# Kernel optimization log

Measured on AMD Instinct MI355X. Metric: run time of the kernel, lower is better.

The kernel has to match this reference:

```python
import jax, jax.numpy as jnp
import numpy as np

NEG = -1000000.0


def setup_inputs() -> dict:
    key = jax.random.key(0)
    k0, k1, k2, k3, k4 = jax.random.split(key, 5)
    b, c, h, w = 4, 256, 64, 64
    dvt_c = 768
    x = jax.random.normal(k0, (b, c, h, w), jnp.float32)
    dvtfeats = jax.random.normal(k1, (b, dvt_c, h, w), jnp.float32)
    coarse = (jax.random.uniform(k2, (b, 1, h, w)) > 0.5).astype(jnp.float32)
    mask = jnp.repeat(jnp.repeat(coarse, 8, axis=2), 8, axis=3)  # [b,1,512,512]
    # K_conv: Conv2d(c+768 -> c, 1x1) with bias; fuse: Conv2d(2c -> c, 1x1) no bias
    K_w = jax.random.normal(k3, (c, c + dvt_c), jnp.float32) * 0.02
    K_b = jnp.zeros((c,), jnp.float32)
    fuse_w = jax.random.normal(k4, (c, 2 * c), jnp.float32) * 0.02
    return {"x": x, "mask": mask, "dvtfeats": dvtfeats, "K_w": K_w, "K_b": K_b, "fuse_w": fuse_w}


def _conv1x1(inp, w, b=None):
    out = jnp.einsum('bihw,oi->bohw', inp, w)
    if b is not None:
        out = out + b[None, :, None, None]
    return out


def _forward(x, mask, dvtfeats, K_w, K_b, fuse_w):
    b, c, h, w = x.shape
    n = h * w
    # maxpool(8,8) then binarize
    m = mask.reshape(b, 1, h, 8, w, 8).max(axis=(3, 5))
    m = (m > 0).astype(x.dtype)            # [b,1,h,w] foreground mask
    bm = 1.0 - m                            # background mask
    # K_conv applied once (original applies the same conv twice to the same input)
    feats = _conv1x1(jnp.concatenate([x, dvtfeats], axis=1), K_w, K_b)  # [b,c,h,w]
    K = (feats * bm).reshape(b, c, n)
    Q = (feats * m).reshape(b, c, n).transpose(0, 2, 1)  # [b,n,c]
    K = K / (jnp.linalg.norm(K, axis=1, keepdims=True) + 1e-8)
    Q = Q / (jnp.linalg.norm(Q, axis=2, keepdims=True) + 1e-8)
    V = (x * bm).reshape(b, c, n)
    score = jnp.einsum('bqc,bck->bqk', Q, K) * 20.0       # [b,n,n] cosine sims
    qm = m.reshape(b, 1, n)    # query mask (foreground)
    km = bm.reshape(b, 1, n)   # key mask (background)
    score = score + (1.0 - km) * NEG + (1.0 - qm).transpose(0, 2, 1) * NEG
    att = jax.nn.softmax(score, axis=-1)
    att = att * qm.transpose(0, 2, 1) * km                # zero out invalid rows/cols
    # att_fore[b,c,q] = sum_k V[b,c,k] * att[b,q,k]
    att_fore = jnp.einsum('bck,bqk->bcq', V, att).reshape(b, c, h, w)
    fused = _conv1x1(jnp.concatenate([att_fore, x], axis=1), fuse_w)
    visatt = att.sum(axis=1).reshape(b, 1, h, w)          # sum over query dim
    attmask = jnp.repeat(jnp.repeat(visatt, 8, axis=2), 8, axis=3)  # nearest upsample x8
    attmask = attmask / attmask.max()
    out = fused * m + x * (1.0 - m)
    return out, attmask


def reference(x, mask, dvtfeats, K_w, K_b, fuse_w):
    return _forward(x, mask, dvtfeats, K_w, K_b, fuse_w)
```

## Files before the change

### kernel.cpp

```cpp
#include <hip/hip_runtime.h>
#include <hip/hip_bf16.h>

typedef __attribute__((ext_vector_type(8))) short short8;
typedef __attribute__((ext_vector_type(4))) float f32x4;
typedef unsigned int uint;
typedef unsigned short ushort;

constexpr int BATCH = 4;
constexpr int CH    = 256;
constexpr int N     = 4096;
constexpr int DVC   = 768;
constexpr int CIN   = 1024;
constexpr int KC    = 512;
constexpr int PBS   = 5 * 1024 * 1024;
constexpr int QCH   = 32;
constexpr int SPLITK = 4;

constexpr size_t OFF_M    = 0;
constexpr size_t OFF_INV  = 64ull << 10;
constexpr size_t OFF_VIS  = 128ull << 10;
constexpr size_t OFF_MAXV = 192ull << 10;
constexpr size_t OFF_CNT  = 196ull << 10;
constexpr size_t OFF_FGI  = 256ull << 10;
constexpr size_t OFF_BGI  = 320ull << 10;
constexpr size_t OFF_P2S  = 384ull << 10;
constexpr size_t OFF_KMC  = 448ull << 10;
constexpr size_t OFF_PART = 1ull << 20;
constexpr size_t OFF_KWB  = 5ull << 20;
constexpr size_t OFF_FWB  = OFF_KWB + (512ull << 10);
constexpr size_t OFF_XT   = 6ull << 20;
constexpr size_t OFF_QC   = 38ull << 20;
constexpr size_t OFF_KCC  = 46ull << 20;
constexpr size_t OFF_XC   = 54ull << 20;
constexpr size_t OFF_AFT  = 62ull << 20;
constexpr size_t OFF_P    = 70ull << 20;
constexpr size_t OFF_AFP  = 110ull << 20;

__device__ __forceinline__ ushort f2bf(float f) {
    __hip_bfloat16 h = __float2bfloat16(f);
    return __builtin_bit_cast(ushort, h);
}
__device__ __forceinline__ float bf2f(ushort u) {
    uint v = (uint)u << 16;
    return __builtin_bit_cast(float, v);
}

typedef const __attribute__((address_space(1))) uint* gptr_t;
typedef __attribute__((address_space(3))) uint* lptr_t;
__device__ __forceinline__ void gload_lds16(const void* g, void* l) {
    __builtin_amdgcn_global_load_lds((gptr_t)g, (lptr_t)l, 16, 0, 0);
}

template<int WM, int WN>
__device__ __forceinline__ void gemm_core(
    const ushort* __restrict__ A0, int lda, int m0,
    const ushort* __restrict__ B0, int ldb0, int kend0,
    const ushort* __restrict__ B1, int ldb1,
    int n0, int K,
    ushort* AsL, ushort* BsL, f32x4 acc[4][4])
{
    constexpr int NW = WM * WN, BM = WM * 64, BN = WN * 64;
    const int t = threadIdx.x, lane = t & 63, wid = t >> 6;
    const int wm = (wid / WN) * 64, wn = (wid % WN) * 64;

    for (int k0 = 0; k0 < K; k0 += 64) {
        #pragma unroll
        for (int c = wid; c < BM / 8; c += NW) {
            const ushort* g = A0 + (size_t)(m0 + c * 8 + (lane >> 3)) * lda + (k0 + (lane & 7) * 8);
            gload_lds16(g, AsL + c * 512);
        }
        const ushort* Bsrc = (k0 < kend0) ? B0 : B1;
        const int ldb = (k0 < kend0) ? ldb0 : ldb1;
        const int kc  = (k0 < kend0) ? k0 : (k0 - kend0);
        #pragma unroll
        for (int c = wid; c < BN / 8; c += NW) {
            const ushort* g = Bsrc + (size_t)(n0 + c * 8 + (lane >> 3)) * ldb + (kc + (lane & 7) * 8);
            gload_lds16(g, BsL + c * 512);
        }
        __syncthreads();

        const int ra = wm + (lane & 15), rb = wn + (lane & 15), ko = (lane >> 4) * 8;
        #pragma unroll
        for (int kk = 0; kk < 64; kk += 32) {
            short8 a[4], b[4];
            #pragma unroll
            for (int i = 0; i < 4; i++) a[i] = *(const short8*)(AsL + (ra + i * 16) * 64 + kk + ko);
            #pragma unroll
            for (int j = 0; j < 4; j++) b[j] = *(const short8*)(BsL + (rb + j * 16) * 64 + kk + ko);
            #pragma unroll
            for (int i = 0; i < 4; i++)
                #pragma unroll
                for (int j = 0; j < 4; j++)
                    acc[i][j] = __builtin_amdgcn_mfma_f32_16x16x32_bf16(a[i], b[j], acc[i][j], 0, 0, 0);
        }
        __syncthreads();
    }
}

__device__ __forceinline__ void zero_acc(f32x4 acc[4][4]) {
    f32x4 z = {0.f, 0.f, 0.f, 0.f};
    #pragma unroll
    for (int i = 0; i < 4; i++)
        #pragma unroll
        for (int j = 0; j < 4; j++) acc[i][j] = z;
}

__global__ __launch_bounds__(256) void k_prep_tr(
    const float* __restrict__ mask, const float* __restrict__ Kw,
    const float* __restrict__ fw, const float* __restrict__ x,
    float* __restrict__ m, float* __restrict__ vis, uint* __restrict__ maxv,
    ushort* __restrict__ Kwb, ushort* __restrict__ fwb, ushort* __restrict__ xT)
{
    __shared__ float Ls[64][65];
    const int bid = blockIdx.x;
    const int t = threadIdx.x;
    if (bid < 64) {
        int idx = bid * 256 + t;
        int b = idx >> 12, p = idx & 4095;
        int y = p >> 6, xx = p & 63;
        const float* base = mask + (size_t)b * 512 * 512 + (y * 8) * 512 + xx * 8;
        float mx = 0.f;
        for (int dy = 0; dy < 8; dy++) {
            #pragma unroll
            for (int dx = 0; dx < 8; dx++) mx = fmaxf(mx, base[dy * 512 + dx]);
        }
        m[idx] = (mx > 0.f) ? 1.f : 0.f;
        vis[idx] = 0.f;
        if (idx == 0) maxv[0] = 0u;
    } else if (bid < 1600) {
        int i = (bid - 64) * 256 + t;
        if (i < CH * CIN) Kwb[i] = f2bf(Kw[i]);
        else              fwb[i - CH * CIN] = f2bf(fw[i - CH * CIN]);
    } else {
        const int tr_id = bid - 1600;
        const int ci0 = (tr_id & 3) * 64;
        const int n0 = ((tr_id >> 2) & 63) * 64;
        const int b = tr_id >> 8;
        const float* s = x + (size_t)b * CH * 4096;
        #pragma unroll
        for (int it = 0; it < 4; it++) {
            int f4 = it * 256 + t;
            int r = f4 >> 4, c4 = f4 & 15;
            float4 v = *(const float4*)(s + (size_t)(ci0 + r) * 4096 + n0 + c4 * 4);
            Ls[r][c4 * 4 + 0] = v.x; Ls[r][c4 * 4 + 1] = v.y;
            Ls[r][c4 * 4 + 2] = v.z; Ls[r][c4 * 4 + 3] = v.w;
        }
        __syncthreads();
        ushort* d = xT + (size_t)b * 4096 * CH;
        #pragma unroll
        for (int it = 0; it < 8; it++) {
            int p = it * 256 + t;
            int rn = p >> 5, cc2 = p & 31;
            uint val = (uint)f2bf(Ls[cc2 * 2][rn]) | ((uint)f2bf(Ls[cc2 * 2 + 1][rn]) << 16);
            *(uint*)(d + (size_t)(n0 + rn) * CH + ci0 + cc2 * 2) = val;
        }
    }
}

__global__ __launch_bounds__(256) void k_scan(
    const float* __restrict__ m, int* __restrict__ fgi, int* __restrict__ bgi,
    int* __restrict__ counts, float* __restrict__ kmc, int* __restrict__ p2s)
{
    const int b = blockIdx.x, t = threadIdx.x;
    const float* mb = m + (size_t)b * N;
    __shared__ int sfg[256], sbg[256];
    bool isf[16];
    int cf = 0, cb_ = 0;
    #pragma unroll
    for (int j = 0; j < 16; j++) {
        bool f = mb[t * 16 + j] != 0.f;
        isf[j] = f; cf += f ? 1 : 0; cb_ += f ? 0 : 1;
    }
    sfg[t] = cf; sbg[t] = cb_;
    __syncthreads();
    for (int off = 1; off < 256; off <<= 1) {
        int vf = (t >= off) ? sfg[t - off] : 0;
        int vb = (t >= off) ? sbg[t - off] : 0;
        __syncthreads();
        sfg[t] += vf; sbg[t] += vb;
        __syncthreads();
    }
    int basef = sfg[t] - cf, baseb = sbg[t] - cb_;
    int nfg = sfg[255], nbg = sbg[255];
    #pragma unroll
    for (int j = 0; j < 16; j++) {
        int p = t * 16 + j;
        if (isf[j]) { fgi[b * N + basef] = p; p2s[b * N + p] = basef | (1 << 30); basef++; }
        else        { bgi[b * N + baseb] = p; p2s[b * N + p] = baseb; baseb++; }
    }
    if (t == 0) {
        counts[b * 4 + 0] = nfg;
        counts[b * 4 + 1] = (nfg + 127) & ~127;
        counts[b * 4 + 2] = nbg;
        counts[b * 4 + 3] = (nbg + 127) & ~127;
    }
    for (int j = t; j < N; j += 256) kmc[b * N + j] = (j < nbg) ? 1.f : 0.f;
}

__global__ __launch_bounds__(256) void k_feats_vg(
    const ushort* __restrict__ Kwb, const ushort* __restrict__ xT,
    const float* __restrict__ dvt, const float* __restrict__ Kb,
    const int* __restrict__ p2s, const int* __restrict__ bgi,
    const int* __restrict__ counts,
    ushort* __restrict__ Qc, ushort* __restrict__ Kc, ushort* __restrict__ xc)
{
    __shared__ __align__(16) char smem[58624];
    const int bid = blockIdx.x;
    const int t = threadIdx.x, lane = t & 63, wid = t >> 6;

    if (bid >= 256) {
        ushort (*Xs)[264] = (ushort(*)[264])smem;
        const int vid = bid - 256;
        const int b = vid >> 6;
        const int ki0 = (vid & 63) * 64;
        const int nbg = counts[b * 4 + 2], nbgp = counts[b * 4 + 3];
        if (ki0 >= nbgp) return;
        const int j = t >> 2, part = t & 3;
        const int ki = ki0 + j;
        if (ki < nbg) {
            const ushort* src = xT + ((size_t)b * N + bgi[(size_t)b * N + ki]) * CH + part * 64;
            #pragma unroll
            for (int q = 0; q < 8; q++)
                *(uint4*)&Xs[j][part * 64 + q * 8] = *(const uint4*)(src + q * 8);
        } else {
            uint4 z = {0, 0, 0, 0};
            #pragma unroll
            for (int q = 0; q < 8; q++)
                *(uint4*)&Xs[j][part * 64 + q * 8] = z;
        }
        __syncthreads();
        const int c = t;
        ushort* dst = xc + ((size_t)b * CH + c) * N + ki0;
        uint w[32];
        #pragma unroll
        for (int jj = 0; jj < 32; jj++)
            w[jj] = (uint)Xs[2 * jj][c] | ((uint)Xs[2 * jj + 1][c] << 16);
        #pragma unroll
        for (int q = 0; q < 8; q++) {
            uint4 o = { w[q * 4], w[q * 4 + 1], w[q * 4 + 2], w[q * 4 + 3] };
            *(uint4*)(dst + q * 8) = o;
        }
        return;
    }

    ushort* As = (ushort*)smem;
    ushort* Bs = (ushort*)(smem + 32768);
    float (*Ls)[65] = (float(*)[65])(smem + 40960);
    float (*red)[64] = (float(*)[64])(smem + 57600);
    const int b = bid >> 6;
    const int n0 = (bid & 63) * 64;
    const ushort* xTb = xT + (size_t)b * N * CH;
    const float* dvb = dvt + (size_t)b * DVC * N;
    f32x4 acc[4][4]; zero_acc(acc);

    for (int k0 = 0; k0 < 256; k0 += 64) {
        #pragma unroll
        for (int c = wid; c < 32; c += 4)
            gload_lds16(Kwb + (size_t)(c * 8 + (lane >> 3)) * CIN + k0 + (lane & 7) * 8, As + c * 512);
        #pragma unroll
        for (int c = wid; c < 8; c += 4)
            gload_lds16(xTb + (size_t)(n0 + c * 8 + (lane >> 3)) * CH + k0 + (lane & 7) * 8, Bs + c * 512);
        __syncthreads();
        const int ra = wid * 64 + (lane & 15), rb = lane & 15, ko = (lane >> 4) * 8;
        #pragma unroll
        for (int kk = 0; kk < 64; kk += 32) {
            short8 a[4], bb[4];
            #pragma unroll
            for (int i = 0; i < 4; i++) a[i] = *(const short8*)(As + (ra + i * 16) * 64 + kk + ko);
            #pragma unroll
            for (int j = 0; j < 4; j++) bb[j] = *(const short8*)(Bs + (rb + j * 16) * 64 + kk + ko);
            #pragma unroll
            for (int i = 0; i < 4; i++)
                #pragma unroll
                for (int j = 0; j < 4; j++)
                    acc[i][j] = __builtin_amdgcn_mfma_f32_16x16x32_bf16(a[i], bb[j], acc[i][j], 0, 0, 0);
        }
        __syncthreads();
    }
    for (int k0 = 256; k0 < 1024; k0 += 64) {
        #pragma unroll
        for (int c = wid; c < 32; c += 4)
            gload_lds16(Kwb + (size_t)(c * 8 + (lane >> 3)) * CIN + k0 + (lane & 7) * 8, As + c * 512);
        const float* dsrc = dvb + (size_t)(k0 - 256) * N + n0;
        #pragma unroll
        for (int it = 0; it < 4; it++) {
            int f4 = it * 256 + t;
            int r = f4 >> 4, c4 = (f4 & 15) * 4;
            float4 v = *(const float4*)(dsrc + (size_t)r * N + c4);
            Ls[r][c4 + 0] = v.x; Ls[r][c4 + 1] = v.y;
            Ls[r][c4 + 2] = v.z; Ls[r][c4 + 3] = v.w;
        }
        __syncthreads();
        {
            int rn = t >> 2;
            int ks = (t & 3) * 16;
            #pragma unroll
            for (int j2 = 0; j2 < 8; j2++) {
                int kk = ks + j2 * 2;
                uint val = (uint)f2bf(Ls[kk][rn]) | ((uint)f2bf(Ls[kk + 1][rn]) << 16);
                int idx = (rn * 64 + kk) ^ ((rn & 7) << 3);
                *(uint*)(Bs + idx) = val;
            }
        }
        __syncthreads();
        const int ra = wid * 64 + (lane & 15), rb = lane & 15, ko = (lane >> 4) * 8;
        #pragma unroll
        for (int kk = 0; kk < 64; kk += 32) {
            short8 a[4], bb[4];
            #pragma unroll
            for (int i = 0; i < 4; i++) a[i] = *(const short8*)(As + (ra + i * 16) * 64 + kk + ko);
            #pragma unroll
            for (int j = 0; j < 4; j++) {
                int row = rb + j * 16;
                int idx = (row * 64 + kk + ko) ^ ((row & 7) << 3);
                bb[j] = *(const short8*)(Bs + idx);
            }
            #pragma unroll
            for (int i = 0; i < 4; i++)
                #pragma unroll
                for (int j = 0; j < 4; j++)
                    acc[i][j] = __builtin_amdgcn_mfma_f32_16x16x32_bf16(a[i], bb[j], acc[i][j], 0, 0, 0);
        }
        __syncthreads();
    }

    const int wm = wid * 64;
    float sj[4] = {0.f, 0.f, 0.f, 0.f};
    #pragma unroll
    for (int i = 0; i < 4; i++) {
        int mbase = wm + i * 16 + ((lane >> 4) * 4);
        float4 bias = *(const float4*)(Kb + mbase);
        #pragma unroll
        for (int j = 0; j < 4; j++) {
            acc[i][j][0] += bias.x; acc[i][j][1] += bias.y;
            acc[i][j][2] += bias.z; acc[i][j][3] += bias.w;
            sj[j] += acc[i][j][0] * acc[i][j][0] + acc[i][j][1] * acc[i][j][1]
                   + acc[i][j][2] * acc[i][j][2] + acc[i][j][3] * acc[i][j][3];
        }
    }
    #pragma unroll
    for (int j = 0; j < 4; j++) {
        sj[j] += __shfl_xor(sj[j], 16);
        sj[j] += __shfl_xor(sj[j], 32);
    }
    if (lane < 16) {
        #pragma unroll
        for (int j = 0; j < 4; j++) red[wid][j * 16 + lane] = sj[j];
    }
    __syncthreads();
    const int* pb = p2s + (size_t)b * N + n0;
    #pragma unroll
    for (int j = 0; j < 4; j++) {
        int n = j * 16 + (lane & 15);
        float s = red[0][n] + red[1][n] + red[2][n] + red[3][n];
        float invn = 1.f / (sqrtf(s) + 1e-8f);
        int sl = pb[n];
        ushort* dst = (sl & (1 << 30)) ? Qc : Kc;
        int slot = sl & 0x3FFFFFFF;
        ushort* drow = dst + ((size_t)b * N + slot) * CH;
        #pragma unroll
        for (int i = 0; i < 4; i++) {
            int mbase = wm + i * 16 + ((lane >> 4) * 4);
            ushort4 o = { f2bf(acc[i][j][0] * invn), f2bf(acc[i][j][1] * invn),
                          f2bf(acc[i][j][2] * invn), f2bf(acc[i][j][3] * invn) };
            *(ushort4*)(drow + mbase) = o;
        }
    }
}

__global__ __launch_bounds__(128) void k_score(
    const ushort* __restrict__ Qc, const ushort* __restrict__ Kc,
    const float* __restrict__ kmc, const int* __restrict__ counts,
    ushort* __restrict__ P, float* __restrict__ rowpart)
{
    const int b = blockIdx.z;
    const int nfgp = counts[b * 4 + 1], nbgp = counts[b * 4 + 3];
    const int m0 = blockIdx.y * 128;
    const int n0 = blockIdx.x * 64;
    if (m0 >= nfgp || n0 >= nbgp) return;
    __shared__ ushort SH[(128 + 64) * 64];
    const int t = threadIdx.x, lane = t & 63, wid = t >> 6;
    const ushort* Qb = Qc + (size_t)b * N * CH;
    const ushort* Kb_ = Kc + (size_t)b * N * CH;
    f32x4 acc[4][4]; zero_acc(acc);
    gemm_core<2, 1>(Qb, CH, m0, Kb_, CH, CH, Kb_, CH, n0, CH, SH, SH + 128 * 64, acc);

    const int wm = wid * 64;
    float km[4];
    #pragma unroll
    for (int j = 0; j < 4; j++) km[j] = kmc[(size_t)b * N + n0 + j * 16 + (lane & 15)];

    ushort* Cs = SH;
    float sir[4][4] = {};
    #pragma unroll
    for (int i = 0; i < 4; i++) {
        int rbase = wm + i * 16 + ((lane >> 4) * 4);
        #pragma unroll
        for (int j = 0; j < 4; j++) {
            int cl = j * 16 + (lane & 15);
            #pragma unroll
            for (int r = 0; r < 4; r++) {
                float p = (km[j] != 0.f) ? __expf(20.f * acc[i][j][r] - 20.f) : 0.f;
                Cs[(rbase + r) * 64 + cl] = f2bf(p);
                sir[i][r] += p;
            }
        }
    }
    #pragma unroll
    for (int i = 0; i < 4; i++)
        #pragma unroll
        for (int r = 0; r < 4; r++) {
            float s = sir[i][r];
            s += __shfl_xor(s, 1); s += __shfl_xor(s, 2);
            s += __shfl_xor(s, 4); s += __shfl_xor(s, 8);
            sir[i][r] = s;
        }
    if ((lane & 15) == 0) {
        const int sl = n0 >> 6;
        #pragma unroll
        for (int i = 0; i < 4; i++)
            #pragma unroll
            for (int r = 0; r < 4; r++) {
                int row = wm + i * 16 + ((lane >> 4) * 4) + r;
                rowpart[((size_t)b * N + m0 + row) * 64 + sl] = sir[i][r];
            }
    }
    __syncthreads();
    ushort* Pb = P + (size_t)b * PBS;
    #pragma unroll
    for (int it = 0; it < 8; it++) {
        int v8 = it * 128 + t;
        int row = v8 >> 3, c8 = (v8 & 7) * 8;
        *(uint4*)(Pb + (size_t)(m0 + row) * nbgp + n0 + c8) = *(const uint4*)(Cs + row * 64 + c8);
    }
}

__global__ __launch_bounds__(256) void k_att_fore(
    const ushort* __restrict__ xc, const ushort* __restrict__ P,
    const int* __restrict__ counts, ushort* __restrict__ AFp)
{
    const int b = blockIdx.z & (BATCH - 1);
    const int sk = blockIdx.z / BATCH;
    const int nfgp = counts[b * 4 + 1], nbgp = counts[b * 4 + 3];
    const int n0 = blockIdx.x * 64;
    if (n0 >= nfgp) return;
    const int kchunk = ((nbgp / 64 + SPLITK - 1) / SPLITK) * 64;
    const int k0s = sk * kchunk;
    const int len = min(kchunk, nbgp - k0s);

    const int lane = threadIdx.x & 63, wid = threadIdx.x >> 6;
    f32x4 acc[4][4]; zero_acc(acc);
    if (len > 0) {
        __shared__ ushort SH[(256 + 64) * 64];
        const ushort* Pb = P + (size_t)b * PBS + k0s;
        gemm_core<4, 1>(xc + (size_t)b * CH * N + k0s, N, 0,
                        Pb, nbgp, 1 << 30, Pb, nbgp,
                        n0, len, SH, SH + 256 * 64, acc);
    }
    ushort* Ap = AFp + ((size_t)(sk * BATCH + b) * N) * CH;
    const int wm = wid * 64;
    #pragma unroll
    for (int j = 0; j < 4; j++) {
        int qi = n0 + j * 16 + (lane & 15);
        #pragma unroll
        for (int i = 0; i < 4; i++) {
            int mbase = wm + i * 16 + ((lane >> 4) * 4);
            ushort4 o = { f2bf(acc[i][j][0]), f2bf(acc[i][j][1]),
                          f2bf(acc[i][j][2]), f2bf(acc[i][j][3]) };
            *(ushort4*)(Ap + (size_t)qi * CH + mbase) = o;
        }
    }
}

__global__ __launch_bounds__(256) void k_rowaf(
    const float* __restrict__ rowpart, const ushort* __restrict__ AFp,
    const int* __restrict__ fgi, const int* __restrict__ counts,
    float* __restrict__ inv, ushort* __restrict__ AFt)
{
    const int t = threadIdx.x, lane = t & 63, wid = t >> 6;
    const int g = blockIdx.x * 4 + wid;
    const int b = g >> 12, qi = g & 4095;
    const int nfgp = counts[b * 4 + 1], nbgp = counts[b * 4 + 3];
    if (qi >= nfgp) return;
    const int nsl = nbgp >> 6;
    float s = (lane < nsl) ? rowpart[(size_t)g * 64 + lane] : 0.f;
    #pragma unroll
    for (int mm = 1; mm < 64; mm <<= 1) s += __shfl_xor(s, mm);
    float iq = (s > 0.f) ? 1.f / s : 0.f;
    if (lane == 0) inv[g] = iq;
    if (qi < counts[b * 4]) {
        const size_t rowoff = ((size_t)b * N + qi) * CH + lane * 4;
        float s0 = 0.f, s1 = 0.f, s2 = 0.f, s3 = 0.f;
        #pragma unroll
        for (int sk = 0; sk < SPLITK; sk++) {
            ushort4 v = *(const ushort4*)(AFp + (size_t)sk * BATCH * N * CH + rowoff);
            s0 += bf2f(v.x); s1 += bf2f(v.y); s2 += bf2f(v.z); s3 += bf2f(v.w);
        }
        int q = fgi[g];
        ushort4 o = { f2bf(s0 * iq), f2bf(s1 * iq), f2bf(s2 * iq), f2bf(s3 * iq) };
        *(ushort4*)(AFt + ((size_t)b * N + q) * CH + lane * 4) = o;
    }
}

__global__ __launch_bounds__(128) void k_fused(
    const ushort* __restrict__ fwb, const ushort* __restrict__ AFt,
    const ushort* __restrict__ xT, const float* __restrict__ x,
    const float* __restrict__ m_, const float* __restrict__ vis,
    const uint* __restrict__ maxv, float* __restrict__ out,
    float* __restrict__ amask)
{
    __shared__ ushort SH[(64 + 128) * 64];
    const int b = blockIdx.z;
    const int n0 = blockIdx.x * 128, m0 = blockIdx.y * 64;
    const int lane = threadIdx.x & 63, wid = threadIdx.x >> 6;
    const int wn = (wid & 1) * 64;
    f32x4 acc[4][4]; zero_acc(acc);
    gemm_core<1, 2>(fwb, KC, m0,
                    AFt + (size_t)b * N * CH, CH, CH,
                    xT + (size_t)b * N * CH, CH,
                    n0, KC, SH, SH + 64 * 64, acc);
    const float* mb = m_ + (size_t)b * N;
    const float* xc_ = x + (size_t)b * CH * N;
    float* ob = out + (size_t)b * CH * N;
    #pragma unroll
    for (int j = 0; j < 4; j++) {
        int n = n0 + wn + j * 16 + (lane & 15);
        float mv = mb[n];
        #pragma unroll
        for (int i = 0; i < 4; i++) {
            int mbase = m0 + i * 16 + ((lane >> 4) * 4);
            #pragma unroll
            for (int r = 0; r < 4; r++) {
                int c = mbase + r;
                ob[(size_t)c * N + n] = (mv != 0.f) ? acc[i][j][r] : xc_[(size_t)c * N + n];
            }
        }
    }
    {
        float rcp = 1.f / __builtin_bit_cast(float, maxv[0]);
        int bid = blockIdx.x + 32 * blockIdx.y + 128 * blockIdx.z;
        int base = bid * 2048;
        #pragma unroll
        for (int it = 0; it < 16; it++) {
            int idx = base + it * 128 + threadIdx.x;
            int bb = idx >> 18;
            int r = idx & 262143;
            int Y = r >> 9, X = r & 511;
            amask[idx] = vis[(size_t)bb * N + (Y >> 3) * 64 + (X >> 3)] * rcp;
        }
    }
}

__global__ __launch_bounds__(256) void k_colsum(
    const ushort* __restrict__ P, const float* __restrict__ inv,
    const int* __restrict__ counts, float* __restrict__ part)
{
    const int b = blockIdx.z, qc = blockIdx.y, t = threadIdx.x;
    const int nfg = counts[b * 4], nbgp = counts[b * 4 + 3];
    const int ki0 = blockIdx.x * 2048 + t * 8;
    if (ki0 >= nbgp) return;
    const int qchunk = (nfg + QCH - 1) / QCH;
    const int q0 = qc * qchunk, q1 = min(q0 + qchunk, nfg);
    const ushort* base = P + (size_t)b * PBS + (size_t)q0 * nbgp + ki0;
    const float* ib = inv + (size_t)b * N;
    float acc[8] = {};
    int q = q0;
    for (; q + 4 <= q1; q += 4) {
        uint4 v0 = *(const uint4*)(base);
        uint4 v1 = *(const uint4*)(base + (size_t)nbgp);
        uint4 v2 = *(const uint4*)(base + 2 * (size_t)nbgp);
        uint4 v3 = *(const uint4*)(base + 3 * (size_t)nbgp);
        float i0 = ib[q], i1 = ib[q + 1], i2 = ib[q + 2], i3 = ib[q + 3];
        const ushort* u0 = (const ushort*)&v0;
        const ushort* u1 = (const ushort*)&v1;
        const ushort* u2 = (const ushort*)&v2;
        const ushort* u3 = (const ushort*)&v3;
        #pragma unroll
        for (int e = 0; e < 8; e++)
            acc[e] += bf2f(u0[e]) * i0 + bf2f(u1[e]) * i1 + bf2f(u2[e]) * i2 + bf2f(u3[e]) * i3;
        base += 4 * (size_t)nbgp;
    }
    for (; q < q1; q++) {
        uint4 v = *(const uint4*)(base);
        float iq = ib[q];
        const ushort* u = (const ushort*)&v;
        #pragma unroll
        for (int e = 0; e < 8; e++) acc[e] += bf2f(u[e]) * iq;
        base += (size_t)nbgp;
    }
    float* pp = part + (size_t)qc * (BATCH * N) + (size_t)b * N + ki0;
    float4 o0 = {acc[0], acc[1], acc[2], acc[3]};
    float4 o1 = {acc[4], acc[5], acc[6], acc[7]};
    *(float4*)(pp)     = o0;
    *(float4*)(pp + 4) = o1;
}

__global__ void k_colsum_final(const float* __restrict__ part, const int* __restrict__ bgi,
                               const int* __restrict__ counts, float* __restrict__ vis,
                               uint* __restrict__ maxv)
{
    int g = blockIdx.x * 256 + threadIdx.x;
    int b = g >> 12, ki = g & 4095;
    int t = threadIdx.x;
    float s = 0.f;
    if (ki < counts[b * 4 + 2]) {
        #pragma unroll
        for (int j = 0; j < QCH; j++) s += part[(size_t)j * (BATCH * N) + g];
        vis[(size_t)b * N + bgi[(size_t)b * N + ki]] = s;
    }
    __shared__ float red[256];
    red[t] = s; __syncthreads();
    for (int st = 128; st > 0; st >>= 1) { if (t < st) red[t] = fmaxf(red[t], red[t + st]); __syncthreads(); }
    if (t == 0) atomicMax(maxv, __float_as_uint(red[0]));
}

extern "C" void kernel_launch(void* const* d_in, const int* in_sizes, int n_in,
                              void* d_out, int out_size, void* d_ws, size_t ws_size,
                              hipStream_t stream)
{
    const float* x    = (const float*)d_in[0];
    const float* mask = (const float*)d_in[1];
    const float* dvt  = (const float*)d_in[2];
    const float* Kw   = (const float*)d_in[3];
    const float* Kb   = (const float*)d_in[4];
    const float* fw   = (const float*)d_in[5];
    float* out = (float*)d_out;

    char* ws = (char*)d_ws;
    float*  m    = (float*)(ws + OFF_M);
    float*  inv  = (float*)(ws + OFF_INV);
    float*  vis  = (float*)(ws + OFF_VIS);
    float*  maxv = (float*)(ws + OFF_MAXV);
    int*    cnt  = (int*)  (ws + OFF_CNT);
    int*    fgi  = (int*)  (ws + OFF_FGI);
    int*    bgi  = (int*)  (ws + OFF_BGI);
    int*    p2s  = (int*)  (ws + OFF_P2S);
    float*  kmc  = (float*)(ws + OFF_KMC);
    float*  part = (float*)(ws + OFF_PART);
    ushort* Kwb  = (ushort*)(ws + OFF_KWB);
    ushort* fwb  = (ushort*)(ws + OFF_FWB);
    ushort* xT   = (ushort*)(ws + OFF_XT);
    ushort* Qc   = (ushort*)(ws + OFF_QC);
    ushort* Kcc  = (ushort*)(ws + OFF_KCC);
    ushort* xc   = (ushort*)(ws + OFF_XC);
    ushort* AFt  = (ushort*)(ws + OFF_AFT);
    ushort* P    = (ushort*)(ws + OFF_P);
    ushort* AFp  = (ushort*)(ws + OFF_AFP);

    k_prep_tr    <<<dim3(1600 + 1024), 256, 0, stream>>>(
                     mask, Kw, fw, x, m, vis, (uint*)maxv, Kwb, fwb, xT);
    k_scan       <<<dim3(BATCH), 256, 0, stream>>>(m, fgi, bgi, cnt, kmc, p2s);
    k_feats_vg   <<<dim3(256 + 256), 256, 0, stream>>>(
                     Kwb, xT, dvt, Kb, p2s, bgi, cnt, Qc, Kcc, xc);
    k_score      <<<dim3(N / 64, N / 128, BATCH), 128, 0, stream>>>(Qc, Kcc, kmc, cnt, P, part);
    k_att_fore   <<<dim3(N / 64, 1, BATCH * SPLITK), 256, 0, stream>>>(xc, P, cnt, AFp);
    k_rowaf      <<<dim3(BATCH * N / 4), 256, 0, stream>>>(part, AFp, fgi, cnt, inv, AFt);
    k_colsum     <<<dim3(2, QCH, BATCH), 256, 0, stream>>>(P, inv, cnt, part);
    k_colsum_final<<<dim3(BATCH * N / 256), 256, 0, stream>>>(part, bgi, cnt, vis, (uint*)maxv);
    k_fused      <<<dim3(N / 128, CH / 64, BATCH), 128, 0, stream>>>(
                     fwb, AFt, xT, x, m, vis, (const uint*)maxv, out, out + (size_t)BATCH * CH * N);
}
```

Baseline: 154.7 us.

## Merge att_fore GEMM and colsum into shared launches after computing row inverses

```diff
diff --git a/kernel.cpp b/kernel.cpp
--- a/kernel.cpp
+++ b/kernel.cpp
@@ -435,47 +435,9 @@
     }
 }
 
-__global__ __launch_bounds__(256) void k_att_fore(
-    const ushort* __restrict__ xc, const ushort* __restrict__ P,
-    const int* __restrict__ counts, ushort* __restrict__ AFp)
-{
-    const int b = blockIdx.z & (BATCH - 1);
-    const int sk = blockIdx.z / BATCH;
-    const int nfgp = counts[b * 4 + 1], nbgp = counts[b * 4 + 3];
-    const int n0 = blockIdx.x * 64;
-    if (n0 >= nfgp) return;
-    const int kchunk = ((nbgp / 64 + SPLITK - 1) / SPLITK) * 64;
-    const int k0s = sk * kchunk;
-    const int len = min(kchunk, nbgp - k0s);
-
-    const int lane = threadIdx.x & 63, wid = threadIdx.x >> 6;
-    f32x4 acc[4][4]; zero_acc(acc);
-    if (len > 0) {
-        __shared__ ushort SH[(256 + 64) * 64];
-        const ushort* Pb = P + (size_t)b * PBS + k0s;
-        gemm_core<4, 1>(xc + (size_t)b * CH * N + k0s, N, 0,
-                        Pb, nbgp, 1 << 30, Pb, nbgp,
-                        n0, len, SH, SH + 256 * 64, acc);
-    }
-    ushort* Ap = AFp + ((size_t)(sk * BATCH + b) * N) * CH;
-    const int wm = wid * 64;
-    #pragma unroll
-    for (int j = 0; j < 4; j++) {
-        int qi = n0 + j * 16 + (lane & 15);
-        #pragma unroll
-        for (int i = 0; i < 4; i++) {
-            int mbase = wm + i * 16 + ((lane >> 4) * 4);
-            ushort4 o = { f2bf(acc[i][j][0]), f2bf(acc[i][j][1]),
-                          f2bf(acc[i][j][2]), f2bf(acc[i][j][3]) };
-            *(ushort4*)(Ap + (size_t)qi * CH + mbase) = o;
-        }
-    }
-}
-
-__global__ __launch_bounds__(256) void k_rowaf(
-    const float* __restrict__ rowpart, const ushort* __restrict__ AFp,
-    const int* __restrict__ fgi, const int* __restrict__ counts,
-    float* __restrict__ inv, ushort* __restrict__ AFt)
+__global__ __launch_bounds__(256) void k_rowinv(
+    const float* __restrict__ rowpart, const int* __restrict__ counts,
+    float* __restrict__ inv)
 {
     const int t = threadIdx.x, lane = t & 63, wid = t >> 6;
     const int g = blockIdx.x * 4 + wid;
@@ -486,20 +448,136 @@
     float s = (lane < nsl) ? rowpart[(size_t)g * 64 + lane] : 0.f;
     #pragma unroll
     for (int mm = 1; mm < 64; mm <<= 1) s += __shfl_xor(s, mm);
-    float iq = (s > 0.f) ? 1.f / s : 0.f;
-    if (lane == 0) inv[g] = iq;
-    if (qi < counts[b * 4]) {
-        const size_t rowoff = ((size_t)b * N + qi) * CH + lane * 4;
-        float s0 = 0.f, s1 = 0.f, s2 = 0.f, s3 = 0.f;
-        #pragma unroll
-        for (int sk = 0; sk < SPLITK; sk++) {
-            ushort4 v = *(const ushort4*)(AFp + (size_t)sk * BATCH * N * CH + rowoff);
-            s0 += bf2f(v.x); s1 += bf2f(v.y); s2 += bf2f(v.z); s3 += bf2f(v.w);
-        }
-        int q = fgi[g];
-        ushort4 o = { f2bf(s0 * iq), f2bf(s1 * iq), f2bf(s2 * iq), f2bf(s3 * iq) };
-        *(ushort4*)(AFt + ((size_t)b * N + q) * CH + lane * 4) = o;
-    }
+    if (lane == 0) inv[g] = (s > 0.f) ? 1.f / s : 0.f;
+}
+
+__global__ __launch_bounds__(256) void k_afc(
+    const ushort* __restrict__ xc, const ushort* __restrict__ P,
+    const float* __restrict__ inv, const int* __restrict__ counts,
+    ushort* __restrict__ AFp, float* __restrict__ part)
+{
+    __shared__ ushort SH[(256 + 64) * 64];
+    const int bid = blockIdx.x;
+    const int t = threadIdx.x;
+
+    if (bid >= 1024) {
+        const int vid = bid - 1024;
+        const int xb = vid & 1;
+        const int qc = (vid >> 1) & 31;
+        const int b = vid >> 6;
+        const int nfg = counts[b * 4], nbgp = counts[b * 4 + 3];
+        const int ki0 = xb * 2048 + t * 8;
+        if (ki0 >= nbgp) return;
+        const int qchunk = (nfg + QCH - 1) / QCH;
+        const int q0 = qc * qchunk, q1 = min(q0 + qchunk, nfg);
+        const ushort* base = P + (size_t)b * PBS + (size_t)q0 * nbgp + ki0;
+        const float* ib = inv + (size_t)b * N;
+        float acc[8] = {};
+        int q = q0;
+        for (; q + 4 <= q1; q += 4) {
+            uint4 v0 = *(const uint4*)(base);
+            uint4 v1 = *(const uint4*)(base + (size_t)nbgp);
+            uint4 v2 = *(const uint4*)(base + 2 * (size_t)nbgp);
+            uint4 v3 = *(const uint4*)(base + 3 * (size_t)nbgp);
+            float i0 = ib[q], i1 = ib[q + 1], i2 = ib[q + 2], i3 = ib[q + 3];
+            const ushort* u0 = (const ushort*)&v0;
+            const ushort* u1 = (const ushort*)&v1;
+            const ushort* u2 = (const ushort*)&v2;
+            const ushort* u3 = (const ushort*)&v3;
+            #pragma unroll
+            for (int e = 0; e < 8; e++)
+                acc[e] += bf2f(u0[e]) * i0 + bf2f(u1[e]) * i1 + bf2f(u2[e]) * i2 + bf2f(u3[e]) * i3;
+            base += 4 * (size_t)nbgp;
+        }
+        for (; q < q1; q++) {
+            uint4 v = *(const uint4*)(base);
+            float iq = ib[q];
+            const ushort* u = (const ushort*)&v;
+            #pragma unroll
+            for (int e = 0; e < 8; e++) acc[e] += bf2f(u[e]) * iq;
+            base += (size_t)nbgp;
+        }
+        float* pp = part + (size_t)qc * (BATCH * N) + (size_t)b * N + ki0;
+        float4 o0 = {acc[0], acc[1], acc[2], acc[3]};
+        float4 o1 = {acc[4], acc[5], acc[6], acc[7]};
+        *(float4*)(pp)     = o0;
+        *(float4*)(pp + 4) = o1;
+        return;
+    }
+
+    const int z = bid >> 6;
+    const int b = z & (BATCH - 1);
+    const int sk = z / BATCH;
+    const int nfgp = counts[b * 4 + 1], nbgp = counts[b * 4 + 3];
+    const int n0 = (bid & 63) * 64;
+    if (n0 >= nfgp) return;
+    const int kchunk = ((nbgp / 64 + SPLITK - 1) / SPLITK) * 64;
+    const int k0s = sk * kchunk;
+    const int len = min(kchunk, nbgp - k0s);
+
+    const int lane = t & 63, wid = t >> 6;
+    f32x4 acc[4][4]; zero_acc(acc);
+    if (len > 0) {
+        const ushort* Pb = P + (size_t)b * PBS + k0s;
+        gemm_core<4, 1>(xc + (size_t)b * CH * N + k0s, N, 0,
+                        Pb, nbgp, 1 << 30, Pb, nbgp,
+                        n0, len, SH, SH + 256 * 64, acc);
+    }
+    ushort* Ap = AFp + ((size_t)(sk * BATCH + b) * N) * CH;
+    const int wm = wid * 64;
+    #pragma unroll
+    for (int j = 0; j < 4; j++) {
+        int qi = n0 + j * 16 + (lane & 15);
+        #pragma unroll
+        for (int i = 0; i < 4; i++) {
+            int mbase = wm + i * 16 + ((lane >> 4) * 4);
+            ushort4 o = { f2bf(acc[i][j][0]), f2bf(acc[i][j][1]),
+                          f2bf(acc[i][j][2]), f2bf(acc[i][j][3]) };
+            *(ushort4*)(Ap + (size_t)qi * CH + mbase) = o;
+        }
+    }
+}
+
+__global__ __launch_bounds__(256) void k_afc_final(
+    const ushort* __restrict__ AFp, const float* __restrict__ inv,
+    const float* __restrict__ part, const int* __restrict__ fgi,
+    const int* __restrict__ bgi, const int* __restrict__ counts,
+    ushort* __restrict__ AFt, float* __restrict__ vis, uint* __restrict__ maxv)
+{
+    __shared__ float red[256];
+    const int bid = blockIdx.x;
+    const int t = threadIdx.x;
+
+    if (bid >= 4096) {
+        int g = (bid - 4096) * 256 + t;
+        int b = g >> 12, ki = g & 4095;
+        float s = 0.f;
+        if (ki < counts[b * 4 + 2]) {
+            #pragma unroll
+            for (int j = 0; j < QCH; j++) s += part[(size_t)j * (BATCH * N) + g];
+            vis[(size_t)b * N + bgi[(size_t)b * N + ki]] = s;
+        }
+        red[t] = s; __syncthreads();
+        for (int st = 128; st > 0; st >>= 1) { if (t < st) red[t] = fmaxf(red[t], red[t + st]); __syncthreads(); }
+        if (t == 0) atomicMax(maxv, __float_as_uint(red[0]));
+        return;
+    }
+
+    const int lane = t & 63, wid = t >> 6;
+    const int g = bid * 4 + wid;
+    const int b = g >> 12, qi = g & 4095;
+    if (qi >= counts[b * 4]) return;
+    const size_t rowoff = ((size_t)b * N + qi) * CH + lane * 4;
+    float s0 = 0.f, s1 = 0.f, s2 = 0.f, s3 = 0.f;
+    #pragma unroll
+    for (int sk = 0; sk < SPLITK; sk++) {
+        ushort4 v = *(const ushort4*)(AFp + (size_t)sk * BATCH * N * CH + rowoff);
+        s0 += bf2f(v.x); s1 += bf2f(v.y); s2 += bf2f(v.z); s3 += bf2f(v.w);
+    }
+    float iq = inv[g];
+    int q = fgi[g];
+    ushort4 o = { f2bf(s0 * iq), f2bf(s1 * iq), f2bf(s2 * iq), f2bf(s3 * iq) };
+    *(ushort4*)(AFt + ((size_t)b * N + q) * CH + lane * 4) = o;
 }
 
 __global__ __launch_bounds__(128) void k_fused(
@@ -549,69 +627,6 @@
             amask[idx] = vis[(size_t)bb * N + (Y >> 3) * 64 + (X >> 3)] * rcp;
         }
     }
-}
-
-__global__ __launch_bounds__(256) void k_colsum(
-    const ushort* __restrict__ P, const float* __restrict__ inv,
-    const int* __restrict__ counts, float* __restrict__ part)
-{
-    const int b = blockIdx.z, qc = blockIdx.y, t = threadIdx.x;
-    const int nfg = counts[b * 4], nbgp = counts[b * 4 + 3];
-    const int ki0 = blockIdx.x * 2048 + t * 8;
-    if (ki0 >= nbgp) return;
-    const int qchunk = (nfg + QCH - 1) / QCH;
-    const int q0 = qc * qchunk, q1 = min(q0 + qchunk, nfg);
-    const ushort* base = P + (size_t)b * PBS + (size_t)q0 * nbgp + ki0;
-    const float* ib = inv + (size_t)b * N;
-    float acc[8] = {};
-    int q = q0;
-    for (; q + 4 <= q1; q += 4) {
-        uint4 v0 = *(const uint4*)(base);
-        uint4 v1 = *(const uint4*)(base + (size_t)nbgp);
-        uint4 v2 = *(const uint4*)(base + 2 * (size_t)nbgp);
-        uint4 v3 = *(const uint4*)(base + 3 * (size_t)nbgp);
-        float i0 = ib[q], i1 = ib[q + 1], i2 = ib[q + 2], i3 = ib[q + 3];
-        const ushort* u0 = (const ushort*)&v0;
-        const ushort* u1 = (const ushort*)&v1;
-        const ushort* u2 = (const ushort*)&v2;
-        const ushort* u3 = (const ushort*)&v3;
-        #pragma unroll
-        for (int e = 0; e < 8; e++)
-            acc[e] += bf2f(u0[e]) * i0 + bf2f(u1[e]) * i1 + bf2f(u2[e]) * i2 + bf2f(u3[e]) * i3;
-        base += 4 * (size_t)nbgp;
-    }
-    for (; q < q1; q++) {
-        uint4 v = *(const uint4*)(base);
-        float iq = ib[q];
-        const ushort* u = (const ushort*)&v;
-        #pragma unroll
-        for (int e = 0; e < 8; e++) acc[e] += bf2f(u[e]) * iq;
-        base += (size_t)nbgp;
-    }
-    float* pp = part + (size_t)qc * (BATCH * N) + (size_t)b * N + ki0;
-    float4 o0 = {acc[0], acc[1], acc[2], acc[3]};
-    float4 o1 = {acc[4], acc[5], acc[6], acc[7]};
-    *(float4*)(pp)     = o0;
-    *(float4*)(pp + 4) = o1;
-}
-
-__global__ void k_colsum_final(const float* __restrict__ part, const int* __restrict__ bgi,
-                               const int* __restrict__ counts, float* __restrict__ vis,
-                               uint* __restrict__ maxv)
-{
-    int g = blockIdx.x * 256 + threadIdx.x;
-    int b = g >> 12, ki = g & 4095;
-    int t = threadIdx.x;
-    float s = 0.f;
-    if (ki < counts[b * 4 + 2]) {
-        #pragma unroll
-        for (int j = 0; j < QCH; j++) s += part[(size_t)j * (BATCH * N) + g];
-        vis[(size_t)b * N + bgi[(size_t)b * N + ki]] = s;
-    }
-    __shared__ float red[256];
-    red[t] = s; __syncthreads();
-    for (int st = 128; st > 0; st >>= 1) { if (t < st) red[t] = fmaxf(red[t], red[t + st]); __syncthreads(); }
-    if (t == 0) atomicMax(maxv, __float_as_uint(red[0]));
 }
 
 extern "C" void kernel_launch(void* const* d_in, const int* in_sizes, int n_in,
@@ -653,10 +668,10 @@
     k_feats_vg   <<<dim3(256 + 256), 256, 0, stream>>>(
                      Kwb, xT, dvt, Kb, p2s, bgi, cnt, Qc, Kcc, xc);
     k_score      <<<dim3(N / 64, N / 128, BATCH), 128, 0, stream>>>(Qc, Kcc, kmc, cnt, P, part);
-    k_att_fore   <<<dim3(N / 64, 1, BATCH * SPLITK), 256, 0, stream>>>(xc, P, cnt, AFp);
-    k_rowaf      <<<dim3(BATCH * N / 4), 256, 0, stream>>>(part, AFp, fgi, cnt, inv, AFt);
-    k_colsum     <<<dim3(2, QCH, BATCH), 256, 0, stream>>>(P, inv, cnt, part);
-    k_colsum_final<<<dim3(BATCH * N / 256), 256, 0, stream>>>(part, bgi, cnt, vis, (uint*)maxv);
+    k_rowinv     <<<dim3(BATCH * N / 4), 256, 0, stream>>>(part, cnt, inv);
+    k_afc        <<<dim3(1024 + 256), 256, 0, stream>>>(xc, P, inv, cnt, AFp, part);
+    k_afc_final  <<<dim3(4096 + 64), 256, 0, stream>>>(
+                     AFp, inv, part, fgi, bgi, cnt, AFt, vis, (uint*)maxv);
     k_fused      <<<dim3(N / 128, CH / 64, BATCH), 128, 0, stream>>>(
                      fwb, AFt, xT, x, m, vis, (const uint*)maxv, out, out + (size_t)BATCH * CH * N);
 }
```

New measurement: 148.4 us. 4.1% less time.
